# Optimization experiments

Measured on AMD Instinct MI355X. Metric: run time of the kernel, lower is better.

## Reference

```python
import jax, jax.numpy as jnp
import numpy as np

B, SQ, C = 8, 4096, 1280
CAD = 2048
H, D = 20, 64          # heads x head_dim = hidden_size
NT = 4                 # num IP tokens
TXT = 77               # text tokens
IP_SCALE = 1.0


def setup_inputs() -> dict:
    key = jax.random.key(0)
    ks = jax.random.split(key, 9)
    s = 0.02
    return {
        "hidden_states": jax.random.normal(ks[0], (B, SQ, C), jnp.float32),
        "encoder_hidden_states": jax.random.normal(ks[1], (B, TXT + NT, CAD), jnp.float32),
        "Wq": jax.random.normal(ks[2], (C, C), jnp.float32) * s,
        "Wk": jax.random.normal(ks[3], (CAD, C), jnp.float32) * s,
        "Wv": jax.random.normal(ks[4], (CAD, C), jnp.float32) * s,
        "Wk_ip": jax.random.normal(ks[5], (CAD, C), jnp.float32) * s,
        "Wv_ip": jax.random.normal(ks[6], (CAD, C), jnp.float32) * s,
        "Wo": jax.random.normal(ks[7], (C, C), jnp.float32) * s,
        "bo": jnp.zeros((C,), jnp.float32),
    }


def _heads(x):
    # [b, s, C] -> [b, H, s, D]
    b, s, _ = x.shape
    return x.reshape(b, s, H, D).transpose(0, 2, 1, 3)


def _attend(q, k, v):
    scale = jnp.asarray(1.0 / np.sqrt(D), q.dtype)
    probs = jax.nn.softmax(jnp.einsum('bhqd,bhkd->bhqk', q, k) * scale, axis=-1)
    return jnp.einsum('bhqk,bhkd->bhqd', probs, v)


def reference(hidden_states, encoder_hidden_states, Wq, Wk, Wv, Wk_ip, Wv_ip, Wo, bo):
    residual = hidden_states
    txt = encoder_hidden_states[:, :-NT, :]   # [B, 77, CAD]
    ip = encoder_hidden_states[:, -NT:, :]    # [B, 4, CAD]

    q = _heads(hidden_states @ Wq)            # [B, H, SQ, D]
    k = _heads(txt @ Wk)
    v = _heads(txt @ Wv)
    out = _attend(q, k, v)                    # text branch

    ip_k = _heads(ip @ Wk_ip)
    ip_v = _heads(ip @ Wv_ip)
    out = out + IP_SCALE * _attend(q, ip_k, ip_v)  # IP-adapter branch

    b = out.shape[0]
    out = out.transpose(0, 2, 1, 3).reshape(b, SQ, C)  # merge heads
    out = out @ Wo + bo
    return out + residual
```

## Files before the change

kernel.cpp:

```cpp
#include <hip/hip_runtime.h>
#include <hip/hip_bf16.h>
#include <cstdint>
#include <cstddef>


typedef __bf16 bf16_t;
typedef __bf16 bf16x8 __attribute__((ext_vector_type(8)));
typedef __bf16 bf16x4 __attribute__((ext_vector_type(4)));
typedef float  f32x4  __attribute__((ext_vector_type(4)));
typedef unsigned int u32x4 __attribute__((ext_vector_type(4)));

using as3_void  = __attribute__((address_space(3))) void;
using as1_cvoid = const __attribute__((address_space(1))) void;

#define TXT_ 77

__device__ __forceinline__ bf16x8 ld16(const void* p) {
  u32x4 v = *(const u32x4*)p;
  return __builtin_bit_cast(bf16x8, v);
}

template <int EPI>
__global__ __launch_bounds__(256, 4)
void gemm_bt(const bf16_t* __restrict__ A, const bf16_t* __restrict__ Bt,
             void* __restrict__ Cout, int ntn, int N, int K,
             const float* __restrict__ bias, const void* __restrict__ residual)
{
  __shared__ __align__(16) char smem[2][16384];
  const int tid  = threadIdx.x;
  const int lane = tid & 63;
  const int wid  = tid >> 6;
  const int wm = wid >> 1, wn = wid & 1;

  const int nwg = gridDim.x;
  int g = blockIdx.x;
  if ((nwg & 7) == 0)
    g = (blockIdx.x & 7) * (nwg >> 3) + (blockIdx.x >> 3);
  const long bm = (long)(g / ntn) * 128;
  const long bn = (long)(g % ntn) * 128;

  f32x4 acc[4][4] = {};

  const int srow = lane >> 2;
  const int skb  = (lane & 3) ^ (((lane >> 2) ^ (lane >> 4)) & 3);
  const int NT = K >> 5;

  auto stage = [&](int buf, int kt) {
    const int k0 = kt << 5;
#pragma unroll
    for (int cc = 0; cc < 2; ++cc) {
      const int c = wid + cc * 4;
      const bf16_t* ga = A + (bm + c * 16 + srow) * (long)K + (k0 + skb * 8);
      __builtin_amdgcn_global_load_lds((as1_cvoid*)ga,
                                       (as3_void*)(&smem[buf][c * 1024]), 16, 0, 0);
      const bf16_t* gb = Bt + (bn + c * 16 + srow) * (long)K + (k0 + skb * 8);
      __builtin_amdgcn_global_load_lds((as1_cvoid*)gb,
                                       (as3_void*)(&smem[buf][8192 + c * 1024]), 16, 0, 0);
    }
  };

  const int rkb    = (((lane >> 4) ^ (lane & 3) ^ ((lane >> 2) & 3)) & 3) << 4;
  const int rrow_a = wm * 64 + (lane & 15);
  const int rrow_b = wn * 64 + (lane & 15);

  stage(0, 0);
  int cur = 0;
  for (int t = 0; t < NT; ++t) {
    __syncthreads();
    if (t + 1 < NT) stage(cur ^ 1, t + 1);
    const char* sa = smem[cur];
    const char* sb = smem[cur] + 8192;
    bf16x8 af[4], bfv[4];
#pragma unroll
    for (int m = 0; m < 4; ++m)
      af[m] = ld16(sa + (rrow_a + m * 16) * 64 + rkb);
#pragma unroll
    for (int n = 0; n < 4; ++n)
      bfv[n] = ld16(sb + (rrow_b + n * 16) * 64 + rkb);
#pragma unroll
    for (int m = 0; m < 4; ++m)
#pragma unroll
      for (int n = 0; n < 4; ++n)
        acc[m][n] = __builtin_amdgcn_mfma_f32_16x16x32_bf16(af[m], bfv[n], acc[m][n], 0, 0, 0);
    cur ^= 1;
  }

  const int orow0 = wm * 64 + ((lane >> 4) << 2);
  const int ocol0 = wn * 64 + (lane & 15);
#pragma unroll
  for (int m = 0; m < 4; ++m) {
#pragma unroll
    for (int n = 0; n < 4; ++n) {
      const long col = bn + ocol0 + n * 16;
#pragma unroll
      for (int r = 0; r < 4; ++r) {
        const long row = bm + orow0 + m * 16 + r;
        if constexpr (EPI == 0) {
          ((bf16_t*)Cout)[row * N + col] = (bf16_t)acc[m][n][r];
        } else {
          ((float*)Cout)[row * N + col] =
              acc[m][n][r] + bias[col] +
              (float)((const bf16_t*)residual)[row * N + col];
        }
      }
    }
  }
}

__global__ __launch_bounds__(256, 3)
void attn_fused(const bf16_t* __restrict__ q, const bf16_t* __restrict__ kvt,
                const bf16_t* __restrict__ kvip, bf16_t* __restrict__ outp)
{
  __shared__ __align__(16) bf16_t K_lds[80 * 64];
  __shared__ __align__(16) bf16_t Kip_lds[16 * 64];
  __shared__ __align__(16) bf16_t Vt_lds[64 * 128];
  __shared__ __align__(16) bf16_t P_lds[4][16 * 128];

  const int tid = threadIdx.x, lane = tid & 63, wid = tid >> 6;
  const int h = blockIdx.y, b = blockIdx.z;
  const int kvcol = h << 6;

  for (int idx = tid; idx < 640; idx += 256) {
    const int j = idx >> 3, c = idx & 7;
    bf16x8 v = {};
    if (j < TXT_) v = ld16(kvt + (long)(b * 80 + j) * 2560 + kvcol + c * 8);
    *(bf16x8*)((char*)K_lds + j * 128 + ((c ^ (j & 7)) << 4)) = v;
  }
  if (tid < 128) {
    const int j = tid >> 3, c = tid & 7;
    bf16x8 v = {};
    if (j < 4) v = ld16(kvip + (long)(b * 4 + j) * 2560 + kvcol + c * 8);
    *(bf16x8*)((char*)Kip_lds + j * 128 + ((c ^ (j & 7)) << 4)) = v;
  }
  for (int idx = tid; idx < 1024; idx += 256) {
    const int key = idx >> 3, c = idx & 7;
    bf16x8 v = {};
    if (key < TXT_)
      v = ld16(kvt + (long)(b * 80 + key) * 2560 + 1280 + kvcol + c * 8);
    else if (key >= 96 && key < 100)
      v = ld16(kvip + (long)(b * 4 + key - 96) * 2560 + 1280 + kvcol + c * 8);
#pragma unroll
    for (int e = 0; e < 8; ++e) {
      const int d = c * 8 + e;
      *(bf16_t*)((char*)Vt_lds + d * 256 + ((key * 2) ^ ((d & 7) << 4))) = v[e];
    }
  }
  for (int idx = tid; idx < 1024; idx += 256)
    *(bf16x8*)((char*)P_lds + idx * 16) = (bf16x8){};
  __syncthreads();

  const int l15 = lane & 15, hi = lane >> 4;
  const int dblk = hi << 3;
  const int prow0 = hi << 2;
  const float scale = 0.125f;
  char* const pw = (char*)P_lds[wid];

  const long qrow0 = (long)b * 4096 + ((long)blockIdx.x << 8) + (wid << 6);
  bf16x8 qf[4][2];
#pragma unroll
  for (int ms = 0; ms < 4; ++ms) {
    const bf16_t* qp = q + (qrow0 + ms * 16 + l15) * 1280 + kvcol;
    qf[ms][0] = ld16(qp + dblk);
    qf[ms][1] = ld16(qp + 32 + dblk);
  }

#pragma unroll
  for (int ms = 0; ms < 4; ++ms) {
    f32x4 sc[5];
#pragma unroll
    for (int t = 0; t < 5; ++t) {
      const int j = (t << 4) + l15;
      const bf16x8 k0 = ld16((char*)K_lds + j * 128 + ((hi ^ (j & 7)) << 4));
      const bf16x8 k1 = ld16((char*)K_lds + j * 128 + (((4 + hi) ^ (j & 7)) << 4));
      f32x4 z = {0.f, 0.f, 0.f, 0.f};
      z = __builtin_amdgcn_mfma_f32_16x16x32_bf16(qf[ms][0], k0, z, 0, 0, 0);
      z = __builtin_amdgcn_mfma_f32_16x16x32_bf16(qf[ms][1], k1, z, 0, 0, 0);
      sc[t] = z;
    }
#pragma unroll
    for (int t = 0; t < 5; ++t) {
      const bool valid = ((t << 4) + l15) < TXT_;
#pragma unroll
      for (int r = 0; r < 4; ++r)
        sc[t][r] = valid ? sc[t][r] * scale : -1e30f;
    }

#pragma unroll
    for (int r = 0; r < 4; ++r) {
      float m = sc[0][r];
#pragma unroll
      for (int t = 1; t < 5; ++t) m = fmaxf(m, sc[t][r]);
      m = fmaxf(m, __shfl_xor(m, 1));
      m = fmaxf(m, __shfl_xor(m, 2));
      m = fmaxf(m, __shfl_xor(m, 4));
      m = fmaxf(m, __shfl_xor(m, 8));
      float l = 0.f;
#pragma unroll
      for (int t = 0; t < 5; ++t) { const float p = __expf(sc[t][r] - m); sc[t][r] = p; l += p; }
      l += __shfl_xor(l, 1);
      l += __shfl_xor(l, 2);
      l += __shfl_xor(l, 4);
      l += __shfl_xor(l, 8);
      const float inv = 1.f / l;
      const int row = prow0 + r;
#pragma unroll
      for (int t = 0; t < 5; ++t)
        *(bf16_t*)(pw + row * 256 + ((((t << 4) + l15) * 2) ^ ((row & 7) << 4))) =
            (bf16_t)(sc[t][r] * inv);
    }

    {
      const bf16x8 ki0 = ld16((char*)Kip_lds + l15 * 128 + ((hi ^ (l15 & 7)) << 4));
      const bf16x8 ki1 = ld16((char*)Kip_lds + l15 * 128 + (((4 + hi) ^ (l15 & 7)) << 4));
      f32x4 z = {0.f, 0.f, 0.f, 0.f};
      z = __builtin_amdgcn_mfma_f32_16x16x32_bf16(qf[ms][0], ki0, z, 0, 0, 0);
      z = __builtin_amdgcn_mfma_f32_16x16x32_bf16(qf[ms][1], ki1, z, 0, 0, 0);
      const bool vip = l15 < 4;
#pragma unroll
      for (int r = 0; r < 4; ++r) {
        const float s = vip ? z[r] * scale : -1e30f;
        float m = s;
        m = fmaxf(m, __shfl_xor(m, 1));
        m = fmaxf(m, __shfl_xor(m, 2));
        m = fmaxf(m, __shfl_xor(m, 4));
        m = fmaxf(m, __shfl_xor(m, 8));
        const float p = __expf(s - m);
        float l = p;
        l += __shfl_xor(l, 1);
        l += __shfl_xor(l, 2);
        l += __shfl_xor(l, 4);
        l += __shfl_xor(l, 8);
        const int row = prow0 + r;
        *(bf16_t*)(pw + row * 256 + (((96 + l15) * 2) ^ ((row & 7) << 4))) =
            (bf16_t)(p * (1.f / l) );
      }
    }

    f32x4 o[4] = {};
#pragma unroll
    for (int s = 0; s < 4; ++s) {
      const bf16x8 pa =
          ld16(pw + l15 * 256 + ((((s << 2) + hi) << 4) ^ ((l15 & 7) << 4)));
#pragma unroll
      for (int n = 0; n < 4; ++n) {
        const int d = (n << 4) + l15;
        const bf16x8 vb =
            ld16((char*)Vt_lds + d * 256 + ((((s << 2) + hi) << 4) ^ ((d & 7) << 4)));
        o[n] = __builtin_amdgcn_mfma_f32_16x16x32_bf16(pa, vb, o[n], 0, 0, 0);
      }
    }

    const long orow = qrow0 + ms * 16 + prow0;
#pragma unroll
    for (int n = 0; n < 4; ++n)
#pragma unroll
      for (int r = 0; r < 4; ++r)
        outp[(orow + r) * 1280 + kvcol + (n << 4) + l15] = (bf16_t)o[n][r];
  }
}

__global__ void cvt_bf16(const float* __restrict__ in, bf16_t* __restrict__ out, long n)
{
  const long i = ((long)blockIdx.x * 256 + threadIdx.x) * 4;
  if (i >= n) return;
  const float4 v = *(const float4*)(in + i);
  bf16x4 r;
  r[0] = (bf16_t)v.x; r[1] = (bf16_t)v.y; r[2] = (bf16_t)v.z; r[3] = (bf16_t)v.w;
  *(bf16x4*)(out + i) = r;
}

__global__ void transpose_cvt(const float* __restrict__ in, bf16_t* __restrict__ out,
                              int K, int N, int ostride)
{
  __shared__ float tile[32][33];
  const int k0 = blockIdx.x * 32, n0 = blockIdx.y * 32;
  for (int i = threadIdx.y; i < 32; i += 8)
    tile[i][threadIdx.x] = in[(long)(k0 + i) * N + n0 + threadIdx.x];
  __syncthreads();
  for (int i = threadIdx.y; i < 32; i += 8)
    out[(long)(n0 + i) * ostride + k0 + threadIdx.x] = (bf16_t)tile[threadIdx.x][i];
}

__global__ void pack_enc(const float* __restrict__ enc, bf16_t* __restrict__ a_txt,
                         bf16_t* __restrict__ a_ip)
{
  const long t4 = ((long)blockIdx.x * 256 + threadIdx.x) * 4;
  const long NTXT = 640L * 2048;
  bf16x4 r;
  r[0] = r[1] = r[2] = r[3] = (bf16_t)0.f;
  if (t4 < NTXT) {
    const int row = (int)(t4 >> 11), col = (int)(t4 & 2047);
    const int b = row / 80, j = row - b * 80;
    if (j < TXT_) {
      const float4 v = *(const float4*)(enc + (((long)(b * 81 + j)) << 11) + col);
      r[0] = (bf16_t)v.x; r[1] = (bf16_t)v.y; r[2] = (bf16_t)v.z; r[3] = (bf16_t)v.w;
    }
    *(bf16x4*)(a_txt + t4) = r;
  } else {
    const long u = t4 - NTXT;
    const int row = (int)(u >> 11), col = (int)(u & 2047);
    if (row < 32) {
      const int b = row >> 2, j = row & 3;
      const float4 v = *(const float4*)(enc + (((long)(b * 81 + TXT_ + j)) << 11) + col);
      r[0] = (bf16_t)v.x; r[1] = (bf16_t)v.y; r[2] = (bf16_t)v.z; r[3] = (bf16_t)v.w;
    }
    *(bf16x4*)(a_ip + u) = r;
  }
}

extern "C" void kernel_launch(void* const* d_in, const int* in_sizes, int n_in,
                              void* d_out, int out_size, void* d_ws, size_t ws_size,
                              hipStream_t stream)
{
  (void)in_sizes; (void)n_in; (void)out_size; (void)ws_size;
  const float* hs  = (const float*)d_in[0];
  const float* enc = (const float*)d_in[1];
  const float* Wq  = (const float*)d_in[2];
  const float* Wk  = (const float*)d_in[3];
  const float* Wv  = (const float*)d_in[4];
  const float* Wki = (const float*)d_in[5];
  const float* Wvi = (const float*)d_in[6];
  const float* Wo  = (const float*)d_in[7];
  const float* bo  = (const float*)d_in[8];

  char* ws = (char*)d_ws;
  size_t off = 0;
  auto alloc = [&](size_t bytes) {
    char* p = ws + off;
    off += (bytes + 255) & ~(size_t)255;
    return p;
  };
  bf16_t* buf1   = (bf16_t*)alloc(83886080);
  bf16_t* qb     = (bf16_t*)alloc(83886080);
  bf16_t* Wq_t   = (bf16_t*)alloc(3276800);
  bf16_t* Wo_t   = (bf16_t*)alloc(3276800);
  bf16_t* Wkv_t  = (bf16_t*)alloc(10485760);
  bf16_t* Wip_t  = (bf16_t*)alloc(10485760);
  bf16_t* a_txt  = (bf16_t*)alloc(2621440);
  bf16_t* a_ip   = (bf16_t*)alloc(524288);
  bf16_t* kv_txt = (bf16_t*)alloc(3276800);
  bf16_t* kv_ip  = (bf16_t*)alloc(655360);

  const dim3 tb(32, 8);
  cvt_bf16<<<40960, 256, 0, stream>>>(hs, buf1, 41943040L);
  transpose_cvt<<<dim3(40, 40), tb, 0, stream>>>(Wq, Wq_t, 1280, 1280, 1280);
  transpose_cvt<<<dim3(40, 40), tb, 0, stream>>>(Wo, Wo_t, 1280, 1280, 1280);
  transpose_cvt<<<dim3(64, 40), tb, 0, stream>>>(Wk, Wkv_t, 2048, 1280, 2048);
  transpose_cvt<<<dim3(64, 40), tb, 0, stream>>>(Wv, Wkv_t + (long)1280 * 2048, 2048, 1280, 2048);
  transpose_cvt<<<dim3(64, 40), tb, 0, stream>>>(Wki, Wip_t, 2048, 1280, 2048);
  transpose_cvt<<<dim3(64, 40), tb, 0, stream>>>(Wvi, Wip_t + (long)1280 * 2048, 2048, 1280, 2048);
  pack_enc<<<1536, 256, 0, stream>>>(enc, a_txt, a_ip);

  gemm_bt<0><<<2560, 256, 0, stream>>>(buf1, Wq_t, qb, 10, 1280, 1280,
                                       nullptr, nullptr);
  gemm_bt<0><<<100, 256, 0, stream>>>(a_txt, Wkv_t, kv_txt, 20, 2560, 2048,
                                      nullptr, nullptr);
  gemm_bt<0><<<20, 256, 0, stream>>>(a_ip, Wip_t, kv_ip, 20, 2560, 2048,
                                     nullptr, nullptr);

  attn_fused<<<dim3(16, 20, 8), 256, 0, stream>>>(qb, kv_txt, kv_ip, qb);

  gemm_bt<2><<<2560, 256, 0, stream>>>(qb, Wo_t, d_out, 10, 1280, 1280,
                                       bo, buf1);
}
```

Baseline: 505.8 us.

## Add 256x256-tile GEMM with 4-stage LDS pipeline for Q and output projections

Adds a new GEMM kernel with 512 threads, 256x256 output tiles and a 4-deep global-to-LDS prefetch ring. It interleaves A and B staging with MFMA phases and raises wave priority around the MFMA blocks. The kernel is used for the large Q projection and the output projection, with the bias+residual epilogue, to cut global traffic per FLOP and hide load latency. The old 128-tile kernel is trimmed to the bf16-only path, used for the small K/V GEMMs, and loses its grid swizzle. The 128KB of LDS limits occupancy to one block per CU. A grid of 640 blocks may also leave some CUs idle in the tail wave.

```diff
diff --git a/kernel.cpp b/kernel.cpp
--- a/kernel.cpp
+++ b/kernel.cpp
@@ -21,10 +21,117 @@
 }
 
 template <int EPI>
+__global__ __launch_bounds__(512, 2)
+void gemm256(const bf16_t* __restrict__ A, const bf16_t* __restrict__ Bt,
+             void* __restrict__ Cout, int ntn, int N, int K,
+             const float* __restrict__ bias, const void* __restrict__ residual)
+{
+  __shared__ __align__(16) char smem[131072];
+  const int tid = threadIdx.x, lane = tid & 63, wid = tid >> 6;
+  const int wm = wid >> 2, wn = wid & 3;
+
+  const int nwg = gridDim.x;
+  int g = blockIdx.x;
+  if ((nwg & 7) == 0) g = (blockIdx.x & 7) * (nwg >> 3) + (blockIdx.x >> 3);
+  const long bm = (long)(g / ntn) * 256;
+  const long bn = (long)(g % ntn) * 256;
+
+  const int NTk = K >> 5;
+
+  const int srow = lane >> 2;
+  const int scol = ((lane & 3) ^ ((lane >> 3) & 3)) * 8;
+
+  auto stageA = [&](int t) {
+    const int buf = t & 3;
+    const long k0 = (long)t << 5;
+#pragma unroll
+    for (int j = 0; j < 2; ++j) {
+      const int ci = j * 8 + wid;
+      const bf16_t* gp = A + (bm + ci * 16 + srow) * (long)K + k0 + scol;
+      __builtin_amdgcn_global_load_lds((as1_cvoid*)gp,
+          (as3_void*)(smem + buf * 16384 + ci * 1024), 16, 0, 0);
+    }
+  };
+  auto stageB = [&](int t) {
+    const int buf = t & 3;
+    const long k0 = (long)t << 5;
+#pragma unroll
+    for (int j = 0; j < 2; ++j) {
+      const int ci = j * 8 + wid;
+      const bf16_t* gp = Bt + (bn + ci * 16 + srow) * (long)K + k0 + scol;
+      __builtin_amdgcn_global_load_lds((as1_cvoid*)gp,
+          (as3_void*)(smem + 65536 + buf * 16384 + ci * 1024), 16, 0, 0);
+    }
+  };
+
+  const int l15 = lane & 15, kq = lane >> 4;
+  const int rc16 = (kq ^ ((l15 >> 1) & 3)) << 4;
+
+  f32x4 acc[8][4] = {};
+
+  stageA(0); stageB(0); stageA(1); stageB(1);
+  asm volatile("s_waitcnt vmcnt(4)" ::: "memory");
+  __builtin_amdgcn_s_barrier();
+
+  for (int t = 0; t < NTk; ++t) {
+    const char* sa = smem + (t & 3) * 16384;
+    const char* sb = smem + 65536 + (t & 3) * 16384;
+    bf16x8 bfr[4], afr[4];
+#pragma unroll
+    for (int n = 0; n < 4; ++n)
+      bfr[n] = ld16(sb + (wn * 64 + n * 16 + l15) * 64 + rc16);
+#pragma unroll
+    for (int m = 0; m < 4; ++m)
+      afr[m] = ld16(sa + (wm * 128 + m * 16 + l15) * 64 + rc16);
+    if (t + 2 < NTk) stageA(t + 2);
+    __builtin_amdgcn_s_setprio(1);
+#pragma unroll
+    for (int m = 0; m < 4; ++m)
+#pragma unroll
+      for (int n = 0; n < 4; ++n)
+        acc[m][n] = __builtin_amdgcn_mfma_f32_16x16x32_bf16(afr[m], bfr[n], acc[m][n], 0, 0, 0);
+    __builtin_amdgcn_s_setprio(0);
+#pragma unroll
+    for (int m = 0; m < 4; ++m)
+      afr[m] = ld16(sa + (wm * 128 + (m + 4) * 16 + l15) * 64 + rc16);
+    if (t + 2 < NTk) stageB(t + 2);
+    __builtin_amdgcn_s_setprio(1);
+#pragma unroll
+    for (int m = 0; m < 4; ++m)
+#pragma unroll
+      for (int n = 0; n < 4; ++n)
+        acc[m + 4][n] = __builtin_amdgcn_mfma_f32_16x16x32_bf16(afr[m], bfr[n], acc[m + 4][n], 0, 0, 0);
+    __builtin_amdgcn_s_setprio(0);
+    if (t == NTk - 2) asm volatile("s_waitcnt vmcnt(0)" ::: "memory");
+    else              asm volatile("s_waitcnt vmcnt(4)" ::: "memory");
+    __builtin_amdgcn_s_barrier();
+    asm volatile("" ::: "memory");
+  }
+
+  const int orow0 = (lane >> 4) << 2;
+#pragma unroll
+  for (int m = 0; m < 8; ++m) {
+#pragma unroll
+    for (int n = 0; n < 4; ++n) {
+      const long col = bn + wn * 64 + n * 16 + l15;
+#pragma unroll
+      for (int r = 0; r < 4; ++r) {
+        const long row = bm + wm * 128 + m * 16 + orow0 + r;
+        if constexpr (EPI == 0) {
+          ((bf16_t*)Cout)[row * N + col] = (bf16_t)acc[m][n][r];
+        } else {
+          ((float*)Cout)[row * N + col] =
+              acc[m][n][r] + bias[col] +
+              (float)((const bf16_t*)residual)[row * N + col];
+        }
+      }
+    }
+  }
+}
+
 __global__ __launch_bounds__(256, 4)
 void gemm_bt(const bf16_t* __restrict__ A, const bf16_t* __restrict__ Bt,
-             void* __restrict__ Cout, int ntn, int N, int K,
-             const float* __restrict__ bias, const void* __restrict__ residual)
+             bf16_t* __restrict__ Cout, int ntn, int N, int K)
 {
   __shared__ __align__(16) char smem[2][16384];
   const int tid  = threadIdx.x;
@@ -32,10 +139,7 @@
   const int wid  = tid >> 6;
   const int wm = wid >> 1, wn = wid & 1;
 
-  const int nwg = gridDim.x;
-  int g = blockIdx.x;
-  if ((nwg & 7) == 0)
-    g = (blockIdx.x & 7) * (nwg >> 3) + (blockIdx.x >> 3);
+  const int g = blockIdx.x;
   const long bm = (long)(g / ntn) * 128;
   const long bn = (long)(g % ntn) * 128;
 
@@ -88,23 +192,14 @@
   const int orow0 = wm * 64 + ((lane >> 4) << 2);
   const int ocol0 = wn * 64 + (lane & 15);
 #pragma unroll
-  for (int m = 0; m < 4; ++m) {
+  for (int m = 0; m < 4; ++m)
 #pragma unroll
     for (int n = 0; n < 4; ++n) {
       const long col = bn + ocol0 + n * 16;
 #pragma unroll
-      for (int r = 0; r < 4; ++r) {
-        const long row = bm + orow0 + m * 16 + r;
-        if constexpr (EPI == 0) {
-          ((bf16_t*)Cout)[row * N + col] = (bf16_t)acc[m][n][r];
-        } else {
-          ((float*)Cout)[row * N + col] =
-              acc[m][n][r] + bias[col] +
-              (float)((const bf16_t*)residual)[row * N + col];
-        }
-      }
-    }
-  }
+      for (int r = 0; r < 4; ++r)
+        Cout[(bm + orow0 + m * 16 + r) * (long)N + col] = (bf16_t)acc[m][n][r];
+    }
 }
 
 __global__ __launch_bounds__(256, 3)
@@ -232,7 +327,7 @@
         l += __shfl_xor(l, 8);
         const int row = prow0 + r;
         *(bf16_t*)(pw + row * 256 + (((96 + l15) * 2) ^ ((row & 7) << 4))) =
-            (bf16_t)(p * (1.f / l) );
+            (bf16_t)(p * (1.f / l));
       }
     }
 
@@ -351,15 +446,13 @@
   transpose_cvt<<<dim3(64, 40), tb, 0, stream>>>(Wvi, Wip_t + (long)1280 * 2048, 2048, 1280, 2048);
   pack_enc<<<1536, 256, 0, stream>>>(enc, a_txt, a_ip);
 
-  gemm_bt<0><<<2560, 256, 0, stream>>>(buf1, Wq_t, qb, 10, 1280, 1280,
-                                       nullptr, nullptr);
-  gemm_bt<0><<<100, 256, 0, stream>>>(a_txt, Wkv_t, kv_txt, 20, 2560, 2048,
+  gemm256<0><<<640, 512, 0, stream>>>(buf1, Wq_t, qb, 5, 1280, 1280,
                                       nullptr, nullptr);
-  gemm_bt<0><<<20, 256, 0, stream>>>(a_ip, Wip_t, kv_ip, 20, 2560, 2048,
-                                     nullptr, nullptr);
+  gemm_bt<<<100, 256, 0, stream>>>(a_txt, Wkv_t, kv_txt, 20, 2560, 2048);
+  gemm_bt<<<20, 256, 0, stream>>>(a_ip, Wip_t, kv_ip, 20, 2560, 2048);
 
   attn_fused<<<dim3(16, 20, 8), 256, 0, stream>>>(qb, kv_txt, kv_ip, qb);
 
-  gemm_bt<2><<<2560, 256, 0, stream>>>(qb, Wo_t, d_out, 10, 1280, 1280,
-                                       bo, buf1);
-}
+  gemm256<2><<<640, 512, 0, stream>>>(qb, Wo_t, d_out, 5, 1280, 1280,
+                                      bo, buf1);
+}
```

Result: faster. 484.8 us (-4.2%).
